# Optimization experiments

Hardware: AMD Instinct MI355X
Metric: run time of the kernel (lower is better)

The kernel has to match this reference:

```python
import jax, jax.numpy as jnp
import numpy as np

GFS = 512   # graph_feat_size
K = 256     # attention dim k
MEAN_MASK_Q = 64.0
MEAN_MASK_A = 64.0


def setup_inputs() -> dict:
    key = jax.random.key(0)
    k1, k2, k3, k4, k5, k6 = jax.random.split(key, 6)
    B, N = 512, 128
    V_n = jax.random.normal(k1, (B, GFS, N), dtype=jnp.float32)
    Q_n = jax.random.normal(k2, (B, GFS, N), dtype=jnp.float32)
    # glorot-uniform-ish init for weights
    def glorot(k, shape):
        lim = np.sqrt(6.0 / (shape[0] + shape[1])).astype(np.float32)
        return jax.random.uniform(k, shape, jnp.float32, -lim, lim)
    W_m = glorot(k3, (K, GFS))
    W_v = glorot(k4, (K, GFS))
    W_q = glorot(k5, (K, GFS))
    W_h = glorot(k6, (1, K))
    return {"V_n": V_n, "Q_n": Q_n, "W_m": W_m, "W_v": W_v, "W_q": W_q, "W_h": W_h}


def reference(V_n, Q_n, W_m, W_v, W_q, W_h):
    # V_n, Q_n: [B, GFS, N]
    V_0 = jnp.tanh(jnp.sum(V_n, axis=-1) / MEAN_MASK_Q)  # [B, GFS]
    Q_0 = jnp.tanh(jnp.sum(Q_n, axis=-1) / MEAN_MASK_A)  # [B, GFS]
    M_0 = V_0 * Q_0                                       # [B, GFS]
    # tanh(W_m @ M_0): [B, K, 1] broadcast over atoms
    m_gate = jnp.tanh(jnp.einsum('kf,bf->bk', W_m, M_0))[:, :, None]  # [B, K, 1]
    H_v = jnp.tanh(jnp.einsum('kf,bfn->bkn', W_v, V_n)) * m_gate      # [B, K, N]
    H_q = jnp.tanh(jnp.einsum('kf,bfn->bkn', W_q, Q_n)) * m_gate      # [B, K, N]
    alpha_v = jax.nn.softmax(jnp.einsum('ok,bkn->bon', W_h, H_v), axis=-1)  # [B, 1, N]
    alpha_q = jax.nn.softmax(jnp.einsum('ok,bkn->bon', W_h, H_q), axis=-1)  # [B, 1, N]
    vector_v = jnp.einsum('bon,bfn->bof', alpha_v, V_n)[:, 0, :]  # [B, GFS]
    vector_q = jnp.einsum('bon,bfn->bof', alpha_q, Q_n)[:, 0, :]  # [B, GFS]
    return vector_v, vector_q, alpha_v, alpha_q
```

## Files before the change

### kernel.cpp

```cpp
#include <hip/hip_runtime.h>
#include <hip/hip_bf16.h>
#include <stdint.h>

#define NBATCH 512
#define FDIM   512
#define NATOM  128
#define KDIM   256
#define NT     16

#define VS_STRIDE 40
#define GV_STRIDE 132

typedef __attribute__((ext_vector_type(8))) __bf16         bf16x8;
typedef __attribute__((ext_vector_type(8))) unsigned short ushort8;
typedef __attribute__((ext_vector_type(4))) float          f32x4;

__device__ __forceinline__ float fast_tanh(float x) {
    float e = __expf(2.0f * x);
    return 1.0f - 2.0f / (e + 1.0f);
}
__device__ __forceinline__ unsigned short bf16_rne(float f) {
    unsigned int u = __float_as_uint(f);
    u += 0x7FFFu + ((u >> 16) & 1u);
    return (unsigned short)(u >> 16);
}
__device__ __forceinline__ float bf16_to_f(unsigned short h) {
    return __uint_as_float(((unsigned int)h) << 16);
}
__device__ __forceinline__ bf16x8 ldfrag(const unsigned short* p) {
    return __builtin_bit_cast(bf16x8, *(const ushort8*)p);
}
__device__ __forceinline__ void glds16(const unsigned short* g, unsigned short* l) {
    __builtin_amdgcn_global_load_lds(
        (const __attribute__((address_space(1))) unsigned int*)g,
        (__attribute__((address_space(3))) unsigned int*)l, 16, 0, 0);
}

__global__ __launch_bounds__(256)
void wconv_kernel(const float* __restrict__ Wv, const float* __restrict__ Wq,
                  unsigned short* __restrict__ out) {
    int i = blockIdx.x * 256 + threadIdx.x;
    int c = i & 3, k = (i >> 2) & 255, s = (i >> 10) & 15, side = i >> 14;
    const float* W = side ? Wq : Wv;
    const float4* p = (const float4*)(W + (size_t)k * FDIM + s * 32 + c * 8);
    float4 a = p[0], b2 = p[1];
    ushort8 o;
    o[0] = bf16_rne(a.x);  o[1] = bf16_rne(a.y);
    o[2] = bf16_rne(a.z);  o[3] = bf16_rne(a.w);
    o[4] = bf16_rne(b2.x); o[5] = bf16_rne(b2.y);
    o[6] = bf16_rne(b2.z); o[7] = bf16_rne(b2.w);
    *(ushort8*)(out + (size_t)i * 8) = o;
}

__global__ __launch_bounds__(1024)
void coattn_kernel(const float* __restrict__ V_n, const float* __restrict__ Q_n,
                   const float* __restrict__ W_m, const float* __restrict__ W_h,
                   const unsigned short* __restrict__ Wt,
                   float* __restrict__ out)
{
    __shared__ unsigned short Ws[2][KDIM * 32];
    __shared__ unsigned short VsT[2][NATOM * VS_STRIDE];
    __shared__ unsigned short Gv[KDIM * GV_STRIDE];
    __shared__ float rsV[FDIM], rsQ[FDIM], m0s[FDIM];
    __shared__ float cgate[KDIM];
    __shared__ float sV[NATOM], sQ[NATOM], alV[NATOM], alQ[NATOM];

    const int b    = blockIdx.x;
    const int t    = threadIdx.x;
    const int lane = t & 63;
    const int wid  = t >> 6;
    const int wr   = wid >> 1;
    const int wc   = wid & 1;
    const int l15  = lane & 15;
    const int lg   = lane >> 4;
    const int fr   = t >> 5;
    const int m    = t & 31;

    const float* Vb = V_n + (size_t)b * FDIM * NATOM;
    const float* Qb = Q_n + (size_t)b * FDIM * NATOM;

    f32x4 acc[2][4];

    const int aoff = (wr * 32 + l15) * 32 + lg * 8;
    const int boff = (wc * 64 + l15) * VS_STRIDE + lg * 8;

    auto stream_gemm = [&](const float* src, const unsigned short* Wside,
                           float* rowsum) {
        {
            f32x4 z = {0.f, 0.f, 0.f, 0.f};
            #pragma unroll
            for (int i = 0; i < 2; ++i)
                #pragma unroll
                for (int j = 0; j < 4; ++j) acc[i][j] = z;
        }
        float vv[2][4];
        auto vload = [&](int s, int buf) {
            const float* p = src + (size_t)(s * 32 + fr) * NATOM + m;
            #pragma unroll
            for (int i = 0; i < 4; ++i) vv[buf][i] = p[32 * i];
        };
        auto vstore = [&](int s, int buf) {
            float rs = vv[buf][0] + vv[buf][1] + vv[buf][2] + vv[buf][3];
            rs += __shfl_xor(rs, 1);
            rs += __shfl_xor(rs, 2);
            rs += __shfl_xor(rs, 4);
            rs += __shfl_xor(rs, 8);
            rs += __shfl_xor(rs, 16);
            if (m == 0) rowsum[s * 32 + fr] = rs;
            #pragma unroll
            for (int i = 0; i < 4; ++i)
                VsT[buf][(m + 32 * i) * VS_STRIDE + fr] = bf16_rne(vv[buf][i]);
        };
        auto wstage = [&](int s, int buf) {
            glds16(Wside + (size_t)s * 8192 + wid * 512 + lane * 8,
                   &Ws[buf][wid * 512]);
        };

        vload(0, 0);
        vstore(0, 0);
        wstage(0, 0);
        vload(1, 1);
        __syncthreads();

        #pragma unroll
        for (int s = 0; s < NT; ++s) {
            const int cur = s & 1;
            bf16x8 af[2], bfr[4];
            #pragma unroll
            for (int mi = 0; mi < 2; ++mi)
                af[mi] = ldfrag(&Ws[cur][aoff + mi * 512]);
            #pragma unroll
            for (int ni = 0; ni < 4; ++ni)
                bfr[ni] = ldfrag(&VsT[cur][boff + ni * 16 * VS_STRIDE]);

            if (s + 2 < NT) vload(s + 2, cur);
            if (s + 1 < NT) { vstore(s + 1, cur ^ 1); wstage(s + 1, cur ^ 1); }

            #pragma unroll
            for (int mi = 0; mi < 2; ++mi)
                #pragma unroll
                for (int ni = 0; ni < 4; ++ni)
                    acc[mi][ni] = __builtin_amdgcn_mfma_f32_16x16x32_bf16(
                        af[mi], bfr[ni], acc[mi][ni], 0, 0, 0);
            __syncthreads();
        }
    };

    stream_gemm(Vb, Wt, rsV);

    #pragma unroll
    for (int mi = 0; mi < 2; ++mi)
        #pragma unroll
        for (int ni = 0; ni < 4; ++ni)
            #pragma unroll
            for (int j = 0; j < 4; ++j) {
                const int k = wr * 32 + mi * 16 + lg * 4 + j;
                const int n = wc * 64 + ni * 16 + l15;
                Gv[k * GV_STRIDE + n] = bf16_rne(fast_tanh(acc[mi][ni][j]));
            }

    stream_gemm(Qb, Wt + 16 * 8192, rsQ);

    __syncthreads();
    if (t < FDIM)
        m0s[t] = fast_tanh(rsV[t] * 0.015625f) * fast_tanh(rsQ[t] * 0.015625f);
    __syncthreads();

    {
        const float4* m04 = (const float4*)m0s;
        float4 mb0 = m04[2 * lane], mb1 = m04[2 * lane + 1];
        #pragma unroll
        for (int kk = wid; kk < KDIM; kk += 16) {
            const float4* wm4 = (const float4*)(W_m + (size_t)kk * FDIM);
            float4 a0 = wm4[2 * lane], a1 = wm4[2 * lane + 1];
            float sum = a0.x*mb0.x + a0.y*mb0.y + a0.z*mb0.z + a0.w*mb0.w
                      + a1.x*mb1.x + a1.y*mb1.y + a1.z*mb1.z + a1.w*mb1.w;
            #pragma unroll
            for (int o = 1; o < 64; o <<= 1) sum += __shfl_xor(sum, o);
            if (lane == 0) cgate[kk] = fast_tanh(sum) * W_h[kk];
        }
    }
    if (t < NATOM) sV[t] = 0.f;
    else if (t < 2 * NATOM) sQ[t - NATOM] = 0.f;
    __syncthreads();

    {
        float sp[4] = {0.f, 0.f, 0.f, 0.f};
        #pragma unroll
        for (int mi = 0; mi < 2; ++mi)
            #pragma unroll
            for (int j = 0; j < 4; ++j) {
                const float c = cgate[wr * 32 + mi * 16 + lg * 4 + j];
                #pragma unroll
                for (int ni = 0; ni < 4; ++ni)
                    sp[ni] += c * fast_tanh(acc[mi][ni][j]);
            }
        #pragma unroll
        for (int ni = 0; ni < 4; ++ni) {
            sp[ni] += __shfl_xor(sp[ni], 16);
            sp[ni] += __shfl_xor(sp[ni], 32);
        }
        if (lg == 0) {
            #pragma unroll
            for (int ni = 0; ni < 4; ++ni)
                atomicAdd(&sQ[wc * 64 + ni * 16 + l15], sp[ni]);
        }
    }
    {
        float s0 = 0.f, s1 = 0.f;
        #pragma unroll
        for (int kk = 0; kk < 16; ++kk) {
            const int k = wid * 16 + kk;
            const float c = cgate[k];
            s0 += c * bf16_to_f(Gv[k * GV_STRIDE + lane]);
            s1 += c * bf16_to_f(Gv[k * GV_STRIDE + 64 + lane]);
        }
        atomicAdd(&sV[lane], s0);
        atomicAdd(&sV[64 + lane], s1);
    }
    __syncthreads();

    if (wid < 2) {
        float* sarr = wid ? sQ : sV;
        float* aarr = wid ? alQ : alV;
        float* oal  = out + 2 * (size_t)NBATCH * FDIM
                    + (size_t)wid * NBATCH * NATOM + (size_t)b * NATOM;
        float a  = sarr[lane];
        float c2 = sarr[64 + lane];
        float mx = fmaxf(a, c2);
        #pragma unroll
        for (int o = 1; o < 64; o <<= 1) mx = fmaxf(mx, __shfl_xor(mx, o));
        float ea = __expf(a - mx), eb = __expf(c2 - mx);
        float ssum = ea + eb;
        #pragma unroll
        for (int o = 1; o < 64; o <<= 1) ssum += __shfl_xor(ssum, o);
        float inv = 1.0f / ssum;
        ea *= inv; eb *= inv;
        aarr[lane] = ea; aarr[64 + lane] = eb;
        oal[lane]  = ea; oal[64 + lane]  = eb;
    }
    __syncthreads();

    {
        float av0 = alV[2 * lane], av1 = alV[2 * lane + 1];
        float aq0 = alQ[2 * lane], aq1 = alQ[2 * lane + 1];
        float* ovV = out + (size_t)b * FDIM;
        float* ovQ = out + (size_t)NBATCH * FDIM + (size_t)b * FDIM;
        #pragma unroll 4
        for (int r = 0; r < 32; ++r) {
            const int f = r * 16 + wid;
            const float2 v2 = *(const float2*)(Vb + (size_t)f * NATOM + 2 * lane);
            const float2 q2 = *(const float2*)(Qb + (size_t)f * NATOM + 2 * lane);
            float sv = v2.x * av0 + v2.y * av1;
            float sq = q2.x * aq0 + q2.y * aq1;
            #pragma unroll
            for (int o = 1; o < 64; o <<= 1) {
                sv += __shfl_xor(sv, o);
                sq += __shfl_xor(sq, o);
            }
            if (lane == 0) { ovV[f] = sv; ovQ[f] = sq; }
        }
    }
}

extern "C" void kernel_launch(void* const* d_in, const int* in_sizes, int n_in,
                              void* d_out, int out_size, void* d_ws, size_t ws_size,
                              hipStream_t stream) {
    (void)in_sizes; (void)n_in; (void)out_size; (void)ws_size;
    const float* V_n = (const float*)d_in[0];
    const float* Q_n = (const float*)d_in[1];
    const float* W_m = (const float*)d_in[2];
    const float* W_v = (const float*)d_in[3];
    const float* W_q = (const float*)d_in[4];
    const float* W_h = (const float*)d_in[5];
    float* out = (float*)d_out;

    unsigned short* Wt = (unsigned short*)d_ws;

    hipLaunchKernelGGL(wconv_kernel, dim3(128), dim3(256), 0, stream,
                       W_v, W_q, Wt);
    hipLaunchKernelGGL(coattn_kernel, dim3(NBATCH), dim3(1024), 0, stream,
                       V_n, Q_n, W_m, W_h, Wt, out);
}
```

Before: 374.0 us.

## Spill V tanh tile to global workspace, reorder prefetch, vectorize final reductions

The bf16 tanh(W_v·V) tile now goes to a per-batch global workspace instead of a large LDS array. This frees about 66KB of LDS so more blocks can be resident, and launch bounds now request higher occupancy. The V-side score is computed with vector loads and 8-lane shuffles, and the gate array is padded. The GEMM loop issues the next stage's stores and loads before the fragment reads, and the final weighted sums use float4 loads with short shuffle reductions. The cost is extra global traffic for the spilled tile, plus register pressure from the stricter launch bounds.

Result: slower. 498.6 us (+33.3%).

```diff
diff --git a/kernel.cpp b/kernel.cpp
--- a/kernel.cpp
+++ b/kernel.cpp
@@ -9,10 +9,12 @@
 #define NT     16
 
 #define VS_STRIDE 40
-#define GV_STRIDE 132
+
+#define CGI(k) ((k) + ((k) >> 5))
 
 typedef __attribute__((ext_vector_type(8))) __bf16         bf16x8;
 typedef __attribute__((ext_vector_type(8))) unsigned short ushort8;
+typedef __attribute__((ext_vector_type(4))) unsigned short ushort4v;
 typedef __attribute__((ext_vector_type(4))) float          f32x4;
 
 __device__ __forceinline__ float fast_tanh(float x) {
@@ -34,6 +36,9 @@
     __builtin_amdgcn_global_load_lds(
         (const __attribute__((address_space(1))) unsigned int*)g,
         (__attribute__((address_space(3))) unsigned int*)l, 16, 0, 0);
+}
+__device__ __forceinline__ float dot4(float4 a, float4 b) {
+    return a.x * b.x + a.y * b.y + a.z * b.z + a.w * b.w;
 }
 
 __global__ __launch_bounds__(256)
@@ -52,17 +57,17 @@
     *(ushort8*)(out + (size_t)i * 8) = o;
 }
 
-__global__ __launch_bounds__(1024)
+__global__ __launch_bounds__(1024, 8)
 void coattn_kernel(const float* __restrict__ V_n, const float* __restrict__ Q_n,
                    const float* __restrict__ W_m, const float* __restrict__ W_h,
                    const unsigned short* __restrict__ Wt,
+                   unsigned short* __restrict__ Gv_ws,
                    float* __restrict__ out)
 {
     __shared__ unsigned short Ws[2][KDIM * 32];
     __shared__ unsigned short VsT[2][NATOM * VS_STRIDE];
-    __shared__ unsigned short Gv[KDIM * GV_STRIDE];
     __shared__ float rsV[FDIM], rsQ[FDIM], m0s[FDIM];
-    __shared__ float cgate[KDIM];
+    __shared__ float cgateP[KDIM + KDIM / 32];
     __shared__ float sV[NATOM], sQ[NATOM], alV[NATOM], alQ[NATOM];
 
     const int b    = blockIdx.x;
@@ -78,6 +83,7 @@
 
     const float* Vb = V_n + (size_t)b * FDIM * NATOM;
     const float* Qb = Q_n + (size_t)b * FDIM * NATOM;
+    unsigned short* Gvb = Gv_ws + (size_t)b * (KDIM * NATOM);
 
     f32x4 acc[2][4];
 
@@ -125,6 +131,9 @@
         #pragma unroll
         for (int s = 0; s < NT; ++s) {
             const int cur = s & 1;
+            if (s + 1 < NT) { vstore(s + 1, cur ^ 1); wstage(s + 1, cur ^ 1); }
+            if (s + 2 < NT) vload(s + 2, cur);
+
             bf16x8 af[2], bfr[4];
             #pragma unroll
             for (int mi = 0; mi < 2; ++mi)
@@ -132,9 +141,6 @@
             #pragma unroll
             for (int ni = 0; ni < 4; ++ni)
                 bfr[ni] = ldfrag(&VsT[cur][boff + ni * 16 * VS_STRIDE]);
-
-            if (s + 2 < NT) vload(s + 2, cur);
-            if (s + 1 < NT) { vstore(s + 1, cur ^ 1); wstage(s + 1, cur ^ 1); }
 
             #pragma unroll
             for (int mi = 0; mi < 2; ++mi)
@@ -151,19 +157,22 @@
     #pragma unroll
     for (int mi = 0; mi < 2; ++mi)
         #pragma unroll
-        for (int ni = 0; ni < 4; ++ni)
-            #pragma unroll
-            for (int j = 0; j < 4; ++j) {
-                const int k = wr * 32 + mi * 16 + lg * 4 + j;
-                const int n = wc * 64 + ni * 16 + l15;
-                Gv[k * GV_STRIDE + n] = bf16_rne(fast_tanh(acc[mi][ni][j]));
-            }
+        for (int ni = 0; ni < 4; ++ni) {
+            ushort4v p;
+            #pragma unroll
+            for (int j = 0; j < 4; ++j)
+                p[j] = bf16_rne(fast_tanh(acc[mi][ni][j]));
+            const int k0 = wr * 32 + mi * 16 + lg * 4;
+            const int n  = wc * 64 + ni * 16 + l15;
+            *(ushort4v*)(Gvb + (size_t)n * KDIM + k0) = p;
+        }
 
     stream_gemm(Qb, Wt + 16 * 8192, rsQ);
 
     __syncthreads();
     if (t < FDIM)
         m0s[t] = fast_tanh(rsV[t] * 0.015625f) * fast_tanh(rsQ[t] * 0.015625f);
+    if (t < NATOM) sQ[t] = 0.f;
     __syncthreads();
 
     {
@@ -173,24 +182,27 @@
         for (int kk = wid; kk < KDIM; kk += 16) {
             const float4* wm4 = (const float4*)(W_m + (size_t)kk * FDIM);
             float4 a0 = wm4[2 * lane], a1 = wm4[2 * lane + 1];
-            float sum = a0.x*mb0.x + a0.y*mb0.y + a0.z*mb0.z + a0.w*mb0.w
-                      + a1.x*mb1.x + a1.y*mb1.y + a1.z*mb1.z + a1.w*mb1.w;
+            float sum = dot4(a0, mb0) + dot4(a1, mb1);
             #pragma unroll
             for (int o = 1; o < 64; o <<= 1) sum += __shfl_xor(sum, o);
-            if (lane == 0) cgate[kk] = fast_tanh(sum) * W_h[kk];
+            if (lane == 0) cgateP[CGI(kk)] = fast_tanh(sum) * W_h[kk];
         }
     }
-    if (t < NATOM) sV[t] = 0.f;
-    else if (t < 2 * NATOM) sQ[t - NATOM] = 0.f;
     __syncthreads();
 
     {
+        const unsigned short* gvp = Gvb + (size_t)(t >> 3) * KDIM + (t & 7) * 32;
+        ushort8 g0 = ((const ushort8*)gvp)[0];
+        ushort8 g1 = ((const ushort8*)gvp)[1];
+        ushort8 g2 = ((const ushort8*)gvp)[2];
+        ushort8 g3 = ((const ushort8*)gvp)[3];
+
         float sp[4] = {0.f, 0.f, 0.f, 0.f};
         #pragma unroll
         for (int mi = 0; mi < 2; ++mi)
             #pragma unroll
             for (int j = 0; j < 4; ++j) {
-                const float c = cgate[wr * 32 + mi * 16 + lg * 4 + j];
+                const float c = cgateP[CGI(wr * 32 + mi * 16 + lg * 4 + j)];
                 #pragma unroll
                 for (int ni = 0; ni < 4; ++ni)
                     sp[ni] += c * fast_tanh(acc[mi][ni][j]);
@@ -205,18 +217,20 @@
             for (int ni = 0; ni < 4; ++ni)
                 atomicAdd(&sQ[wc * 64 + ni * 16 + l15], sp[ni]);
         }
-    }
-    {
-        float s0 = 0.f, s1 = 0.f;
-        #pragma unroll
-        for (int kk = 0; kk < 16; ++kk) {
-            const int k = wid * 16 + kk;
-            const float c = cgate[k];
-            s0 += c * bf16_to_f(Gv[k * GV_STRIDE + lane]);
-            s1 += c * bf16_to_f(Gv[k * GV_STRIDE + 64 + lane]);
-        }
-        atomicAdd(&sV[lane], s0);
-        atomicAdd(&sV[64 + lane], s1);
+
+        const int kb = (t & 7) * 32;
+        float pv = 0.f;
+        #pragma unroll
+        for (int i = 0; i < 8; ++i) {
+            pv += cgateP[CGI(kb + i)]      * bf16_to_f((unsigned short)g0[i]);
+            pv += cgateP[CGI(kb + 8 + i)]  * bf16_to_f((unsigned short)g1[i]);
+            pv += cgateP[CGI(kb + 16 + i)] * bf16_to_f((unsigned short)g2[i]);
+            pv += cgateP[CGI(kb + 24 + i)] * bf16_to_f((unsigned short)g3[i]);
+        }
+        pv += __shfl_xor(pv, 1);
+        pv += __shfl_xor(pv, 2);
+        pv += __shfl_xor(pv, 4);
+        if ((t & 7) == 0) sV[t >> 3] = pv;
     }
     __syncthreads();
 
@@ -242,23 +256,35 @@
     __syncthreads();
 
     {
-        float av0 = alV[2 * lane], av1 = alV[2 * lane + 1];
-        float aq0 = alQ[2 * lane], aq1 = alQ[2 * lane + 1];
+        const int fo = t >> 3;
+        const int n4 = (t & 7) * 4;
+        const float4* alv4 = (const float4*)alV;
+        float4 av0 = alv4[n4], av1 = alv4[n4 + 1], av2 = alv4[n4 + 2], av3 = alv4[n4 + 3];
         float* ovV = out + (size_t)b * FDIM;
+        #pragma unroll
+        for (int pass = 0; pass < 4; ++pass) {
+            const int f = pass * 128 + fo;
+            const float4* vp = (const float4*)(Vb + (size_t)f * NATOM + n4 * 4);
+            float s = dot4(vp[0], av0) + dot4(vp[1], av1)
+                    + dot4(vp[2], av2) + dot4(vp[3], av3);
+            s += __shfl_xor(s, 1);
+            s += __shfl_xor(s, 2);
+            s += __shfl_xor(s, 4);
+            if ((t & 7) == 0) ovV[f] = s;
+        }
+        const float4* alq4 = (const float4*)alQ;
+        float4 aq0 = alq4[n4], aq1 = alq4[n4 + 1], aq2 = alq4[n4 + 2], aq3 = alq4[n4 + 3];
         float* ovQ = out + (size_t)NBATCH * FDIM + (size_t)b * FDIM;
-        #pragma unroll 4
-        for (int r = 0; r < 32; ++r) {
-            const int f = r * 16 + wid;
-            const float2 v2 = *(const float2*)(Vb + (size_t)f * NATOM + 2 * lane);
-            const float2 q2 = *(const float2*)(Qb + (size_t)f * NATOM + 2 * lane);
-            float sv = v2.x * av0 + v2.y * av1;
-            float sq = q2.x * aq0 + q2.y * aq1;
-            #pragma unroll
-            for (int o = 1; o < 64; o <<= 1) {
-                sv += __shfl_xor(sv, o);
-                sq += __shfl_xor(sq, o);
-            }
-            if (lane == 0) { ovV[f] = sv; ovQ[f] = sq; }
+        #pragma unroll
+        for (int pass = 0; pass < 4; ++pass) {
+            const int f = pass * 128 + fo;
+            const float4* qp = (const float4*)(Qb + (size_t)f * NATOM + n4 * 4);
+            float s = dot4(qp[0], aq0) + dot4(qp[1], aq1)
+                    + dot4(qp[2], aq2) + dot4(qp[3], aq3);
+            s += __shfl_xor(s, 1);
+            s += __shfl_xor(s, 2);
+            s += __shfl_xor(s, 4);
+            if ((t & 7) == 0) ovQ[f] = s;
         }
     }
 }
@@ -275,10 +301,11 @@
     const float* W_h = (const float*)d_in[5];
     float* out = (float*)d_out;
 
-    unsigned short* Wt = (unsigned short*)d_ws;
+    unsigned short* Wt    = (unsigned short*)d_ws;
+    unsigned short* Gv_ws = Wt + 2 * 16 * 8192;
 
     hipLaunchKernelGGL(wconv_kernel, dim3(128), dim3(256), 0, stream,
                        W_v, W_q, Wt);
     hipLaunchKernelGGL(coattn_kernel, dim3(NBATCH), dim3(1024), 0, stream,
-                       V_n, Q_n, W_m, W_h, Wt, out);
-}
+                       V_n, Q_n, W_m, W_h, Wt, Gv_ws, out);
+}
```
